# Kernel optimization log

Measured on AMD Instinct MI355X. Metric: run time of the kernel, lower is better.

## Reference

```python
import jax, jax.numpy as jnp
import numpy as np

NEG_BIG = -9e15
ALPHA = 0.2  # LeakyReLU negative slope


def setup_inputs() -> dict:
    key = jax.random.key(0)
    k_h, k_adj, k_W, k_a = jax.random.split(key, 4)
    B, N, F_in, F_out = 16, 2048, 128, 64
    h = jax.random.normal(k_h, (B, N, F_in), dtype=jnp.float32)
    adj = jax.random.randint(k_adj, (B, N, N), 0, 2).astype(jnp.float32)
    mask = jnp.ones((B, N, 1), dtype=jnp.float32)
    W = jax.random.normal(k_W, (F_in, F_out), dtype=jnp.float32) * (1.0 / np.sqrt(F_in))
    a = jax.random.normal(k_a, (2 * F_out, 1), dtype=jnp.float32) * (1.0 / np.sqrt(2 * F_out))
    return {"h": h, "adj": adj, "mask": mask, "W": W, "a": a}


def reference(h, adj, mask, W, a):
    # h: [B,N,Fi], adj: [B,N,N], mask: [B,N,1], W: [Fi,Fo], a: [2Fo,1]
    F_out = W.shape[1]
    Wh = jnp.einsum("bnf,fo->bno", h, W)  # [B,N,Fo]
    # concat(Wh_i, Wh_j) @ a == (Wh @ a_src)_i + (Wh @ a_dst)_j  -- avoids O(B N^2 2Fo) tensor
    a_src = a[:F_out, 0]
    a_dst = a[F_out:, 0]
    f_i = Wh @ a_src  # [B,N]
    f_j = Wh @ a_dst  # [B,N]
    e = jax.nn.leaky_relu(f_i[:, :, None] + f_j[:, None, :], negative_slope=ALPHA)  # [B,N,N]
    node_mask = mask[..., 0]  # [B,N]
    edge_mask = (adj > 0).astype(e.dtype) * node_mask[:, None, :] * node_mask[:, :, None]
    attn_logits = jnp.where(edge_mask > 0, e, jnp.full_like(e, NEG_BIG))
    attention = jax.nn.softmax(attn_logits, axis=2)  # dropout p=0 -> identity
    h_prime = jnp.einsum("bij,bjo->bio", attention, Wh)  # [B,N,Fo]
    return jax.nn.relu(h_prime)
```

## Files before the change

### kernel.cpp

```cpp
#include <hip/hip_runtime.h>
#include <stdint.h>


#define BB   16
#define NN   2048
#define FIN  128
#define FO   64
#define LOG2E 1.4426950408889634f

typedef float v4f __attribute__((ext_vector_type(4)));
typedef short v8s __attribute__((ext_vector_type(8)));
typedef int   v4i __attribute__((ext_vector_type(4)));

__device__ __forceinline__ int pack_bf16(float e0, float e1) {
    unsigned u0 = __float_as_uint(e0) + 0x8000u;
    unsigned u1 = __float_as_uint(e1) + 0x8000u;
    return (int)__builtin_amdgcn_perm(u1, u0, 0x07060302u);
}

__global__ __launch_bounds__(128) void k_wh(
    const float* __restrict__ h, const float* __restrict__ W,
    const float* __restrict__ a,
    float* __restrict__ fsl2, float* __restrict__ fdl2,
    unsigned short* __restrict__ whT)
{
    __shared__ float Wlds[FIN * FO];
    __shared__ float hs[64 * 129];

    const int t  = threadIdx.x;
    const int b  = blockIdx.y;
    const int n0 = blockIdx.x * 64;

    {
        const v4f* Wg = (const v4f*)W;
        v4f* Wl = (v4f*)Wlds;
        #pragma unroll
        for (int i = 0; i < 16; ++i) Wl[t + 128 * i] = Wg[t + 128 * i];
    }
    {
        const v4f* hg = (const v4f*)(h + ((size_t)b * NN + n0) * FIN);
        #pragma unroll
        for (int i = 0; i < 16; ++i) {
            int idx = t + 128 * i;
            v4f v = __builtin_nontemporal_load(hg + idx);
            int r = idx >> 5;
            int c = (idx & 31) * 4;
            float* d = &hs[r * 129 + c];
            d[0] = v[0]; d[1] = v[1]; d[2] = v[2]; d[3] = v[3];
        }
    }
    __syncthreads();

    const int rg = t & 15;
    const int og = t >> 4;

    float acc[4][8];
    #pragma unroll
    for (int r = 0; r < 4; ++r)
        #pragma unroll
        for (int k = 0; k < 8; ++k) acc[r][k] = 0.f;

    #pragma unroll 2
    for (int f = 0; f < FIN; ++f) {
        float hv[4];
        #pragma unroll
        for (int r = 0; r < 4; ++r) hv[r] = hs[(rg * 4 + r) * 129 + f];
        const v4f* wr = (const v4f*)&Wlds[f * FO + og * 8];
        v4f w0 = wr[0];
        v4f w1 = wr[1];
        #pragma unroll
        for (int r = 0; r < 4; ++r) {
            acc[r][0] += hv[r] * w0[0]; acc[r][1] += hv[r] * w0[1];
            acc[r][2] += hv[r] * w0[2]; acc[r][3] += hv[r] * w0[3];
            acc[r][4] += hv[r] * w1[0]; acc[r][5] += hv[r] * w1[1];
            acc[r][6] += hv[r] * w1[2]; acc[r][7] += hv[r] * w1[3];
        }
    }

    float fs[4] = {0.f, 0.f, 0.f, 0.f};
    float fd[4] = {0.f, 0.f, 0.f, 0.f};
    #pragma unroll
    for (int k = 0; k < 8; ++k) {
        float as = a[og * 8 + k];
        float ad = a[FO + og * 8 + k];
        #pragma unroll
        for (int r = 0; r < 4; ++r) {
            fs[r] += acc[r][k] * as;
            fd[r] += acc[r][k] * ad;
        }
    }
    __syncthreads();
    #pragma unroll
    for (int r = 0; r < 4; ++r) {
        hs[og * 64 + rg * 4 + r]       = fs[r];
        hs[512 + og * 64 + rg * 4 + r] = fd[r];
    }
    __syncthreads();
    if (t < 64) {
        float s = 0.f, d2 = 0.f;
        #pragma unroll
        for (int g = 0; g < 8; ++g) {
            s  += hs[g * 64 + t];
            d2 += hs[512 + g * 64 + t];
        }
        fsl2[b * NN + n0 + t] = s  * LOG2E;
        fdl2[b * NN + n0 + t] = d2 * LOG2E;
    }

    #pragma unroll
    for (int k = 0; k < 8; ++k) {
        int o = og * 8 + k;
        int2 pk;
        pk.x = pack_bf16(acc[0][k], acc[1][k]);
        pk.y = pack_bf16(acc[2][k], acc[3][k]);
        *(int2*)&whT[((size_t)b * FO + o) * NN + n0 + rg * 4] = pk;
    }
}

__global__ __launch_bounds__(256) void k_attn(
    const float* __restrict__ adj, const float* __restrict__ fsl2,
    const float* __restrict__ fdl2,
    const unsigned short* __restrict__ whT, float* __restrict__ out)
{
    const int t    = threadIdx.x;
    const int lane = t & 63;
    const int wv   = t >> 6;
    const int lin  = blockIdx.x;
    const int xcd  = lin & 7;
    const int s    = lin >> 3;
    const int b    = xcd * 2 + (s >> 5);
    const int itile = s & 31;
    const int i_base = itile * 64 + wv * 16;
    const int m    = lane & 15;
    const int quad = lane >> 4;

    const float fil2 = fsl2[b * NN + i_base + m];

    const float* adjrow = adj + ((size_t)(b * NN + i_base + m)) * NN + quad * 8;
    const float* fdp = fdl2 + b * NN + quad * 8;
    const unsigned short* wbse = whT + (size_t)b * FO * NN + quad * 8;
    const unsigned short* wp0 = wbse + (size_t)(m     ) * NN;
    const unsigned short* wp1 = wbse + (size_t)(m + 16) * NN;
    const unsigned short* wp2 = wbse + (size_t)(m + 32) * NN;
    const unsigned short* wp3 = wbse + (size_t)(m + 48) * NN;

    v4i onesi = {0x3F803F80, 0x3F803F80, 0x3F803F80, 0x3F803F80};
    v8s onesf = __builtin_bit_cast(v8s, onesi);

    v4f acc0 = {0.f, 0.f, 0.f, 0.f};
    v4f acc1 = {0.f, 0.f, 0.f, 0.f};
    v4f acc2 = {0.f, 0.f, 0.f, 0.f};
    v4f acc3 = {0.f, 0.f, 0.f, 0.f};
    v4f accs = {0.f, 0.f, 0.f, 0.f};

    #pragma unroll 4
    for (int j0 = 0; j0 < NN; j0 += 32) {
        v4f A0 = __builtin_nontemporal_load((const v4f*)(adjrow + j0));
        v4f A1 = __builtin_nontemporal_load((const v4f*)(adjrow + j0 + 4));
        v4f F0 = *(const v4f*)(fdp + j0);
        v4f F1 = *(const v4f*)(fdp + j0 + 4);
        v8s b0 = *(const v8s*)(wp0 + j0);
        v8s b1 = *(const v8s*)(wp1 + j0);
        v8s b2 = *(const v8s*)(wp2 + j0);
        v8s b3 = *(const v8s*)(wp3 + j0);

        float w[8];
        #pragma unroll
        for (int e = 0; e < 8; ++e) {
            float av = (e < 4) ? A0[e] : A1[e - 4];
            float fv = (e < 4) ? F0[e] : F1[e - 4];
            float sc = fil2 + fv;
            float lr = fmaxf(sc, 0.2f * sc);
            w[e] = av * __builtin_amdgcn_exp2f(lr);
        }
        v4i pk;
        pk.x = pack_bf16(w[0], w[1]);
        pk.y = pack_bf16(w[2], w[3]);
        pk.z = pack_bf16(w[4], w[5]);
        pk.w = pack_bf16(w[6], w[7]);
        v8s afrag = __builtin_bit_cast(v8s, pk);

        acc0 = __builtin_amdgcn_mfma_f32_16x16x32_bf16(afrag, b0, acc0, 0, 0, 0);
        acc1 = __builtin_amdgcn_mfma_f32_16x16x32_bf16(afrag, b1, acc1, 0, 0, 0);
        acc2 = __builtin_amdgcn_mfma_f32_16x16x32_bf16(afrag, b2, acc2, 0, 0, 0);
        acc3 = __builtin_amdgcn_mfma_f32_16x16x32_bf16(afrag, b3, acc3, 0, 0, 0);
        accs = __builtin_amdgcn_mfma_f32_16x16x32_bf16(afrag, onesf, accs, 0, 0, 0);
    }

    #pragma unroll
    for (int r = 0; r < 4; ++r) {
        float l = accs[r];
        float inv = l > 0.f ? 1.0f / l : 0.f;
        size_t ro = ((size_t)(b * NN + i_base + quad * 4 + r)) * FO + m;
        __builtin_nontemporal_store(fmaxf(acc0[r] * inv, 0.f), out + ro);
        __builtin_nontemporal_store(fmaxf(acc1[r] * inv, 0.f), out + ro + 16);
        __builtin_nontemporal_store(fmaxf(acc2[r] * inv, 0.f), out + ro + 32);
        __builtin_nontemporal_store(fmaxf(acc3[r] * inv, 0.f), out + ro + 48);
    }
}

extern "C" void kernel_launch(void* const* d_in, const int* in_sizes, int n_in,
                              void* d_out, int out_size, void* d_ws, size_t ws_size,
                              hipStream_t stream)
{
    const float* h   = (const float*)d_in[0];
    const float* adj = (const float*)d_in[1];
    const float* W   = (const float*)d_in[3];
    const float* a   = (const float*)d_in[4];
    float* out = (float*)d_out;

    char* ws = (char*)d_ws;
    float* fsl2 = (float*)ws;
    float* fdl2 = (float*)(ws + 131072);
    unsigned short* whT = (unsigned short*)(ws + 262144);

    k_wh  <<<dim3(NN / 64, BB), 128, 0, stream>>>(h, W, a, fsl2, fdl2, whT);
    k_attn<<<dim3(512),         256, 0, stream>>>(adj, fsl2, fdl2, whT, out);
}
```

Baseline: 419.6 us.

## Compress adjacency to bitmask in prekernel and stage Wh through LDS pipeline

The first kernel now also converts the fp32 adjacency matrix into a packed bitmask using wave ballots. It runs on blocks that are interleaved with the Wh-projection blocks. The attention kernel then reads the compact mask and fdl2 from LDS. It streams Wh^T tiles into a triple-buffered LDS ring with async global_load_lds and manual waitcnt and barriers. The full adjacency read still happens once, but it moves out of the MFMA loop, which removes per-block redundant global traffic. This adds an extra kernel pass over adj and more complex synchronisation.

```diff
diff --git a/kernel.cpp b/kernel.cpp
--- a/kernel.cpp
+++ b/kernel.cpp
@@ -7,29 +7,101 @@
 #define FIN  128
 #define FO   64
 #define LOG2E 1.4426950408889634f
+#define NWORDS 1048576
+#define NGFULL 87381
 
 typedef float v4f __attribute__((ext_vector_type(4)));
 typedef short v8s __attribute__((ext_vector_type(8)));
 typedef int   v4i __attribute__((ext_vector_type(4)));
+typedef unsigned int u32;
+typedef unsigned long long u64;
 
 __device__ __forceinline__ int pack_bf16(float e0, float e1) {
-    unsigned u0 = __float_as_uint(e0) + 0x8000u;
-    unsigned u1 = __float_as_uint(e1) + 0x8000u;
-    return (int)__builtin_amdgcn_perm(u1, u0, 0x07060302u);
-}
-
-__global__ __launch_bounds__(128) void k_wh(
+    unsigned a0 = __float_as_uint(e0) + 0x8000u;
+    unsigned a1 = __float_as_uint(e1) + 0x8000u;
+    return (int)__builtin_amdgcn_perm(a1, a0, 0x07060302u);
+}
+
+__device__ __forceinline__ void gload16(const void* g, void* l) {
+    __builtin_amdgcn_global_load_lds(
+        (const __attribute__((address_space(1))) u32*)g,
+        (__attribute__((address_space(3))) u32*)l, 16, 0, 0);
+}
+
+__global__ __launch_bounds__(128) void k_pre(
     const float* __restrict__ h, const float* __restrict__ W,
-    const float* __restrict__ a,
+    const float* __restrict__ a, const float* __restrict__ adj,
     float* __restrict__ fsl2, float* __restrict__ fdl2,
-    unsigned short* __restrict__ whT)
+    unsigned short* __restrict__ whT, u64* __restrict__ mask)
 {
     __shared__ float Wlds[FIN * FO];
     __shared__ float hs[64 * 129];
 
-    const int t  = threadIdx.x;
-    const int b  = blockIdx.y;
-    const int n0 = blockIdx.x * 64;
+    const int bid = blockIdx.x;
+    const int t   = threadIdx.x;
+
+    if ((bid & 3) != 0) {
+        const int cid = bid - (bid >> 2) - 1;
+        const int wid = cid * 2 + (t >> 6);
+        const int l   = t & 63;
+
+        for (int g = wid; g < NGFULL; g += 3072) {
+            const float* p = adj + (size_t)g * 768 + l;
+            float f0  = __builtin_nontemporal_load(p);
+            float f1  = __builtin_nontemporal_load(p + 64);
+            float f2  = __builtin_nontemporal_load(p + 128);
+            float f3  = __builtin_nontemporal_load(p + 192);
+            float f4  = __builtin_nontemporal_load(p + 256);
+            float f5  = __builtin_nontemporal_load(p + 320);
+            float f6  = __builtin_nontemporal_load(p + 384);
+            float f7  = __builtin_nontemporal_load(p + 448);
+            float f8  = __builtin_nontemporal_load(p + 512);
+            float f9  = __builtin_nontemporal_load(p + 576);
+            float f10 = __builtin_nontemporal_load(p + 640);
+            float f11 = __builtin_nontemporal_load(p + 704);
+            u64 b0  = __ballot(f0  != 0.0f);
+            u64 b1  = __ballot(f1  != 0.0f);
+            u64 b2  = __ballot(f2  != 0.0f);
+            u64 b3  = __ballot(f3  != 0.0f);
+            u64 b4  = __ballot(f4  != 0.0f);
+            u64 b5  = __ballot(f5  != 0.0f);
+            u64 b6  = __ballot(f6  != 0.0f);
+            u64 b7  = __ballot(f7  != 0.0f);
+            u64 b8  = __ballot(f8  != 0.0f);
+            u64 b9  = __ballot(f9  != 0.0f);
+            u64 b10 = __ballot(f10 != 0.0f);
+            u64 b11 = __ballot(f11 != 0.0f);
+            if (l == 0) {
+                v4i* mp = (v4i*)((char*)mask + (size_t)g * 96);
+                v4i s0 = {(int)(u32)b0,  (int)(b0  >> 32), (int)(u32)b1,  (int)(b1  >> 32)};
+                v4i s1 = {(int)(u32)b2,  (int)(b2  >> 32), (int)(u32)b3,  (int)(b3  >> 32)};
+                v4i s2 = {(int)(u32)b4,  (int)(b4  >> 32), (int)(u32)b5,  (int)(b5  >> 32)};
+                v4i s3 = {(int)(u32)b6,  (int)(b6  >> 32), (int)(u32)b7,  (int)(b7  >> 32)};
+                v4i s4 = {(int)(u32)b8,  (int)(b8  >> 32), (int)(u32)b9,  (int)(b9  >> 32)};
+                v4i s5 = {(int)(u32)b10, (int)(b10 >> 32), (int)(u32)b11, (int)(b11 >> 32)};
+                mp[0] = s0; mp[1] = s1; mp[2] = s2;
+                mp[3] = s3; mp[4] = s4; mp[5] = s5;
+            }
+        }
+        if (cid == 0 && (t >> 6) == 0) {
+            const float* p = adj + (size_t)NGFULL * 768 + l;
+            u64 b0 = __ballot(__builtin_nontemporal_load(p)       != 0.0f);
+            u64 b1 = __ballot(__builtin_nontemporal_load(p + 64)  != 0.0f);
+            u64 b2 = __ballot(__builtin_nontemporal_load(p + 128) != 0.0f);
+            u64 b3 = __ballot(__builtin_nontemporal_load(p + 192) != 0.0f);
+            if (l == 0) {
+                v4i* mp = (v4i*)((char*)mask + (size_t)NGFULL * 96);
+                v4i s0 = {(int)(u32)b0, (int)(b0 >> 32), (int)(u32)b1, (int)(b1 >> 32)};
+                v4i s1 = {(int)(u32)b2, (int)(b2 >> 32), (int)(u32)b3, (int)(b3 >> 32)};
+                mp[0] = s0; mp[1] = s1;
+            }
+        }
+        return;
+    }
+
+    const int tile = bid >> 2;
+    const int b  = tile >> 5;
+    const int n0 = (tile & 31) * 64;
 
     {
         const v4f* Wg = (const v4f*)W;
@@ -118,10 +190,12 @@
 }
 
 __global__ __launch_bounds__(256) void k_attn(
-    const float* __restrict__ adj, const float* __restrict__ fsl2,
-    const float* __restrict__ fdl2,
-    const unsigned short* __restrict__ whT, float* __restrict__ out)
+    const u64* __restrict__ mask, const float* __restrict__ fsl2,
+    const float* __restrict__ fdl2, const unsigned short* __restrict__ whT,
+    float* __restrict__ out)
 {
+    __shared__ char smem[49664];
+
     const int t    = threadIdx.x;
     const int lane = t & 63;
     const int wv   = t >> 6;
@@ -133,16 +207,40 @@
     const int i_base = itile * 64 + wv * 16;
     const int m    = lane & 15;
     const int quad = lane >> 4;
+    const int l    = lane;
 
     const float fil2 = fsl2[b * NN + i_base + m];
-
-    const float* adjrow = adj + ((size_t)(b * NN + i_base + m)) * NN + quad * 8;
-    const float* fdp = fdl2 + b * NN + quad * 8;
-    const unsigned short* wbse = whT + (size_t)b * FO * NN + quad * 8;
-    const unsigned short* wp0 = wbse + (size_t)(m     ) * NN;
-    const unsigned short* wp1 = wbse + (size_t)(m + 16) * NN;
-    const unsigned short* wp2 = wbse + (size_t)(m + 32) * NN;
-    const unsigned short* wp3 = wbse + (size_t)(m + 48) * NN;
+    {
+        const v4f* fg = (const v4f*)(fdl2 + b * NN);
+        v4f* fl = (v4f*)smem;
+        fl[t]       = fg[t];
+        fl[t + 256] = fg[t + 256];
+    }
+    {
+        const u64* mg = mask + (size_t)b * 65536 + itile * 2048;
+        #pragma unroll
+        for (int k = 0; k < 8; ++k) {
+            int g = k * 256 + t;
+            *(u64*)(smem + 8192 + (g >> 5) * 264 + (g & 31) * 8) = mg[g];
+        }
+    }
+
+    const unsigned short* wg = whT + (size_t)b * FO * NN
+        + (size_t)(wv * 16 + (l >> 2)) * NN + ((l & 3) ^ (l >> 4)) * 8;
+    char* Wr = smem + 25088;
+    const int wdst = wv * 1024 + l * 16;
+
+#define STAGE_W(cn, base_) do {                              \
+        gload16(wg + (cn) * 64,      (base_) + wdst);        \
+        gload16(wg + (cn) * 64 + 32, (base_) + 4096 + wdst); \
+    } while (0)
+
+    STAGE_W(0, Wr);
+    STAGE_W(1, Wr + 8192);
+    __syncthreads();
+
+    const int pw0  = m * 64 + (quad ^ (m >> 2)) * 16;
+    const int bitb = 8192 + (wv * 16 + m) * 264 + quad;
 
     v4i onesi = {0x3F803F80, 0x3F803F80, 0x3F803F80, 0x3F803F80};
     v8s onesf = __builtin_bit_cast(v8s, onesi);
@@ -153,44 +251,61 @@
     v4f acc3 = {0.f, 0.f, 0.f, 0.f};
     v4f accs = {0.f, 0.f, 0.f, 0.f};
 
-    #pragma unroll 4
-    for (int j0 = 0; j0 < NN; j0 += 32) {
-        v4f A0 = __builtin_nontemporal_load((const v4f*)(adjrow + j0));
-        v4f A1 = __builtin_nontemporal_load((const v4f*)(adjrow + j0 + 4));
-        v4f F0 = *(const v4f*)(fdp + j0);
-        v4f F1 = *(const v4f*)(fdp + j0 + 4);
-        v8s b0 = *(const v8s*)(wp0 + j0);
-        v8s b1 = *(const v8s*)(wp1 + j0);
-        v8s b2 = *(const v8s*)(wp2 + j0);
-        v8s b3 = *(const v8s*)(wp3 + j0);
-
-        float w[8];
-        #pragma unroll
-        for (int e = 0; e < 8; ++e) {
-            float av = (e < 4) ? A0[e] : A1[e - 4];
-            float fv = (e < 4) ? F0[e] : F1[e - 4];
-            float sc = fil2 + fv;
-            float lr = fmaxf(sc, 0.2f * sc);
-            w[e] = av * __builtin_amdgcn_exp2f(lr);
-        }
-        v4i pk;
-        pk.x = pack_bf16(w[0], w[1]);
-        pk.y = pack_bf16(w[2], w[3]);
-        pk.z = pack_bf16(w[4], w[5]);
-        pk.w = pack_bf16(w[6], w[7]);
-        v8s afrag = __builtin_bit_cast(v8s, pk);
-
-        acc0 = __builtin_amdgcn_mfma_f32_16x16x32_bf16(afrag, b0, acc0, 0, 0, 0);
-        acc1 = __builtin_amdgcn_mfma_f32_16x16x32_bf16(afrag, b1, acc1, 0, 0, 0);
-        acc2 = __builtin_amdgcn_mfma_f32_16x16x32_bf16(afrag, b2, acc2, 0, 0, 0);
-        acc3 = __builtin_amdgcn_mfma_f32_16x16x32_bf16(afrag, b3, acc3, 0, 0, 0);
-        accs = __builtin_amdgcn_mfma_f32_16x16x32_bf16(afrag, onesf, accs, 0, 0, 0);
-    }
+    int rd = 0, wr = 16384;
+
+    for (int c = 0; c < 32; ++c) {
+        if (c < 31) asm volatile("s_waitcnt vmcnt(2)" ::: "memory");
+        else        asm volatile("s_waitcnt vmcnt(0)" ::: "memory");
+        __builtin_amdgcn_s_barrier();
+        __builtin_amdgcn_sched_barrier(0);
+        if (c < 30) STAGE_W(c + 2, Wr + wr);
+        __builtin_amdgcn_sched_barrier(0);
+
+        const char* wb = Wr + rd;
+
+        #pragma unroll
+        for (int ks = 0; ks < 2; ++ks) {
+            unsigned bmb = *(const unsigned char*)(smem + bitb + c * 8 + ks * 4);
+            v4f F0 = *(const v4f*)(smem + c * 256 + ks * 128 + quad * 32);
+            v4f F1 = *(const v4f*)(smem + c * 256 + ks * 128 + quad * 32 + 16);
+
+            float w[8];
+            #pragma unroll
+            for (int e = 0; e < 8; ++e) {
+                float fv = (e < 4) ? F0[e] : F1[e - 4];
+                float sc = fil2 + fv;
+                float lr = fmaxf(sc, 0.2f * sc);
+                float ex = __builtin_amdgcn_exp2f(lr);
+                w[e] = (bmb & (1u << e)) ? ex : 0.0f;
+            }
+            v4i pk;
+            pk.x = pack_bf16(w[0], w[1]);
+            pk.y = pack_bf16(w[2], w[3]);
+            pk.z = pack_bf16(w[4], w[5]);
+            pk.w = pack_bf16(w[6], w[7]);
+            v8s afrag = __builtin_bit_cast(v8s, pk);
+
+            v8s b0 = *(const v8s*)(wb + ks * 4096 + pw0);
+            v8s b1 = *(const v8s*)(wb + ks * 4096 + pw0 + 1024);
+            v8s b2 = *(const v8s*)(wb + ks * 4096 + pw0 + 2048);
+            v8s b3 = *(const v8s*)(wb + ks * 4096 + pw0 + 3072);
+
+            acc0 = __builtin_amdgcn_mfma_f32_16x16x32_bf16(afrag, b0, acc0, 0, 0, 0);
+            acc1 = __builtin_amdgcn_mfma_f32_16x16x32_bf16(afrag, b1, acc1, 0, 0, 0);
+            acc2 = __builtin_amdgcn_mfma_f32_16x16x32_bf16(afrag, b2, acc2, 0, 0, 0);
+            acc3 = __builtin_amdgcn_mfma_f32_16x16x32_bf16(afrag, b3, acc3, 0, 0, 0);
+            accs = __builtin_amdgcn_mfma_f32_16x16x32_bf16(afrag, onesf, accs, 0, 0, 0);
+        }
+
+        rd += 8192; if (rd == 24576) rd = 0;
+        wr += 8192; if (wr == 24576) wr = 0;
+    }
+#undef STAGE_W
 
     #pragma unroll
     for (int r = 0; r < 4; ++r) {
-        float l = accs[r];
-        float inv = l > 0.f ? 1.0f / l : 0.f;
+        float dl = accs[r];
+        float inv = dl > 0.f ? 1.0f / dl : 0.f;
         size_t ro = ((size_t)(b * NN + i_base + quad * 4 + r)) * FO + m;
         __builtin_nontemporal_store(fmaxf(acc0[r] * inv, 0.f), out + ro);
         __builtin_nontemporal_store(fmaxf(acc1[r] * inv, 0.f), out + ro + 16);
@@ -213,7 +328,8 @@
     float* fsl2 = (float*)ws;
     float* fdl2 = (float*)(ws + 131072);
     unsigned short* whT = (unsigned short*)(ws + 262144);
-
-    k_wh  <<<dim3(NN / 64, BB), 128, 0, stream>>>(h, W, a, fsl2, fdl2, whT);
-    k_attn<<<dim3(512),         256, 0, stream>>>(adj, fsl2, fdl2, whT, out);
-}
+    u64* mask = (u64*)(ws + 4456448);
+
+    k_pre <<<dim3(2048), 128, 0, stream>>>(h, W, a, adj, fsl2, fdl2, whT, mask);
+    k_attn<<<dim3(512),  256, 0, stream>>>(mask, fsl2, fdl2, whT, out);
+}
```

Measured after the change: 433.4 us. 1.03x slower.
